# Optimization experiments

Hardware: AMD Instinct MI355X
Metric: run time of the kernel (lower is better)

The kernel has to match this reference:

```python
import jax, jax.numpy as jnp
import numpy as np

N = 20000   # nodes
E = 320000  # edges (before self loops)
B = 32      # graphs in batch
H = 4       # heads
C = 64      # per-head channels
NEG_SLOPE = 0.2


def setup_inputs() -> dict:
    key = jax.random.key(0)
    ks = jax.random.split(key, 16)
    x = jax.random.normal(ks[0], (N, 62), jnp.float32)
    pos = jax.random.uniform(ks[1], (N, 2), jnp.float32)
    edge_index = jax.random.randint(ks[2], (2, E), 0, N, jnp.int64)
    batch = jnp.sort(jax.random.randint(ks[3], (N,), 0, B, jnp.int64))
    def glorot(k, shape):
        fan = shape[0] + shape[-1]
        return jax.random.normal(k, shape, jnp.float32) * jnp.sqrt(2.0 / fan)
    # GAT layer 1: in 64 -> H*C = 256
    W1 = glorot(ks[4], (64, H * C))
    a_src1 = glorot(ks[5], (H, C))
    a_dst1 = glorot(ks[6], (H, C))
    b1 = jnp.zeros((H * C,), jnp.float32)
    # GAT layer 2: in 256 -> 256
    W2 = glorot(ks[7], (H * C, H * C))
    a_src2 = glorot(ks[8], (H, C))
    a_dst2 = glorot(ks[9], (H, C))
    b2 = jnp.zeros((H * C,), jnp.float32)
    # linear tail 256 -> 128 -> 10
    lw1 = glorot(ks[10], (H * C, 128))
    lb1 = jnp.zeros((128,), jnp.float32)
    lw2 = glorot(ks[11], (128, 10))
    lb2 = jnp.zeros((10,), jnp.float32)
    return {"x": x, "pos": pos, "edge_index": edge_index, "batch": batch,
            "W1": W1, "a_src1": a_src1, "a_dst1": a_dst1, "b1": b1,
            "W2": W2, "a_src2": a_src2, "a_dst2": a_dst2, "b2": b2,
            "lw1": lw1, "lb1": lb1, "lw2": lw2, "lb2": lb2}


def gat_layer(x, src, dst, W, a_src, a_dst, b):
    # x: [N, F_in] -> h: [N, H, C]
    h = (x @ W).reshape(N, H, C)
    alpha_s = jnp.einsum('nhc,hc->nh', h, a_src)  # [N,H]
    alpha_d = jnp.einsum('nhc,hc->nh', h, a_dst)
    e = alpha_s[src] + alpha_d[dst]               # [E',H]
    e = jax.nn.leaky_relu(e, NEG_SLOPE)
    # softmax over incoming edges per destination node
    emax = jax.ops.segment_max(e, dst, num_segments=N)  # every node has a self loop
    p = jnp.exp(e - emax[dst])
    denom = jax.ops.segment_sum(p, dst, num_segments=N)
    alpha = p / (denom[dst] + 1e-16)              # [E',H]
    msg = h[src] * alpha[..., None]               # [E',H,C] gather + weight
    out = jax.ops.segment_sum(msg, dst, num_segments=N)  # scatter-add
    return out.reshape(N, H * C) + b


def reference(x, pos, edge_index, batch, W1, a_src1, a_dst1, b1,
              W2, a_src2, a_dst2, b2, lw1, lb1, lw2, lb2):
    out = jnp.concatenate([pos, x], axis=1)       # [N, 64]
    loop = jnp.arange(N, dtype=edge_index.dtype)
    src = jnp.concatenate([edge_index[0], loop])  # add self loops (PyG default)
    dst = jnp.concatenate([edge_index[1], loop])
    out = gat_layer(out, src, dst, W1, a_src1, a_dst1, b1)
    out = gat_layer(out, src, dst, W2, a_src2, a_dst2, b2)
    # global mean pool per graph
    sums = jax.ops.segment_sum(out, batch, num_segments=B)
    cnt = jax.ops.segment_sum(jnp.ones((N, 1), out.dtype), batch, num_segments=B)
    out = sums / jnp.maximum(cnt, 1.0)            # [B, 256]
    # dropout(p=0.2) is identity in eval mode
    out = jax.nn.relu(out @ lw1 + lb1)
    out = jax.nn.relu(out @ lw2 + lb2)            # relu after every linear, incl. last (faithful)
    return out
```

## Files before the change

### kernel.cpp

```cpp
#include <hip/hip_runtime.h>
#include <hip/hip_bf16.h>
#include <math.h>

#define N_NODES 20000
#define N_EDGES 320000
#define N_EDGES_SL (N_EDGES + N_NODES)
#define NB 32
#define NH 4
#define HC 256
#define POOL_CH 20
#define DCAP 64

typedef short s16x8 __attribute__((ext_vector_type(8)));
typedef unsigned short u16x8 __attribute__((ext_vector_type(8)));
typedef float f32x4 __attribute__((ext_vector_type(4)));

__device__ __forceinline__ float bf2f(ushort u) {
    union { unsigned int i; float f; } v; v.i = ((unsigned int)u) << 16; return v.f;
}
__device__ __forceinline__ ushort f2bf(float f) {
    union { float f; unsigned int i; } v; v.f = f;
    unsigned int u = v.i;
    unsigned int r = (u + 0x7FFFu + ((u >> 16) & 1u)) >> 16;
    return (ushort)r;
}

#define NZERO (N_NODES + NB * HC)
#define PB_ZERO   ((NZERO + 255) / 256)
#define PB_CONCAT 5000
#define PB_TCONV1 64
#define PB_TCONV2 256
__global__ __launch_bounds__(256) void prep_kernel(const float* __restrict__ x,
                                                   const float* __restrict__ pos,
                                                   ushort* __restrict__ x0,
                                                   const float* __restrict__ W1,
                                                   ushort* __restrict__ Wt1,
                                                   const float* __restrict__ W2,
                                                   ushort* __restrict__ Wt2,
                                                   int* __restrict__ fillc,
                                                   float* __restrict__ poolsum,
                                                   const int* __restrict__ batch,
                                                   int* __restrict__ gstart) {
    int blk = blockIdx.x;
    if (blk < PB_ZERO) {
        int i = blk * 256 + threadIdx.x;
        if (i < N_NODES) fillc[i] = 0;
        else if (i < NZERO) poolsum[i - N_NODES] = 0.f;
    } else if (blk < PB_ZERO + PB_CONCAT) {
        int i = (blk - PB_ZERO) * 256 + threadIdx.x;
        int n = i >> 6, j = i & 63;
        float v = (j < 2) ? pos[n * 2 + j] : x[n * 62 + (j - 2)];
        x0[i] = f2bf(v);
    } else if (blk < PB_ZERO + PB_CONCAT + PB_TCONV1) {
        int i = (blk - PB_ZERO - PB_CONCAT) * 256 + threadIdx.x;
        int n = i >> 6, k = i & 63;
        Wt1[i] = f2bf(W1[k * 256 + n]);
    } else if (blk < PB_ZERO + PB_CONCAT + PB_TCONV1 + PB_TCONV2) {
        int i = (blk - PB_ZERO - PB_CONCAT - PB_TCONV1) * 256 + threadIdx.x;
        int n = i >> 8, k = i & 255;
        Wt2[i] = f2bf(W2[k * 256 + n]);
    } else {
        int t = threadIdx.x;
        if (t > NB) return;
        int lo = 0, hi = N_NODES;
        while (lo < hi) {
            int mid = (lo + hi) >> 1;
            if (batch[mid] < t) lo = mid + 1; else hi = mid;
        }
        gstart[t] = lo;
    }
}

#define PB_FILL ((N_EDGES_SL + 255) / 256)
template<int K, int KC, bool DOFILL>
__global__ __launch_bounds__(256) void mfma_gemm(const ushort* __restrict__ A,
                                                 const ushort* __restrict__ Bt,
                                                 ushort* __restrict__ C,
                                                 const float* __restrict__ a_src,
                                                 const float* __restrict__ a_dst,
                                                 float* __restrict__ asb,
                                                 float* __restrict__ adb,
                                                 const int* __restrict__ ei,
                                                 int* __restrict__ fillc,
                                                 int* __restrict__ srclist) {
    constexpr int KP = KC + 8;
    constexpr int GEMM_BLOCKS = 2 * ((N_NODES + 63) / 64);
    int t = blockIdx.x;
    if (DOFILL && t >= GEMM_BLOCKS) {
        int i = (t - GEMM_BLOCKS) * 256 + threadIdx.x;
        if (i < N_EDGES_SL) {
            int src, dst;
            if (i < N_EDGES) { src = ei[i]; dst = ei[N_EDGES + i]; }
            else             { src = i - N_EDGES; dst = src; }
            int slot = atomicAdd(&fillc[dst], 1);
            if (slot < DCAP) srclist[dst * DCAP + slot] = src;
        }
        return;
    }
    __shared__ __align__(16) ushort As[64 * KP];
    __shared__ __align__(16) ushort Bs[128 * KP];
    int tid = threadIdx.x;
    int col0 = (t & 1) * 128, row0 = (t >> 1) * 64;
    int wave = tid >> 6, lane = tid & 63;
    int mm = lane & 15, quad = lane >> 4;
    f32x4 acc[8] = {};

    for (int kc0 = 0; kc0 < K; kc0 += KC) {
        if (kc0) __syncthreads();
        constexpr int ITER_A = (64 * KC) / 2048;
        constexpr int ITER_B = (128 * KC) / 2048;
#pragma unroll
        for (int it = 0; it < ITER_A; ++it) {
            int f = it * 2048 + tid * 8;
            int r = f / KC, k = f - r * KC;
            uint4 av = make_uint4(0u, 0u, 0u, 0u);
            if (row0 + r < N_NODES) av = *(const uint4*)&A[(size_t)(row0 + r) * K + kc0 + k];
            *(uint4*)&As[r * KP + k] = av;
        }
#pragma unroll
        for (int it = 0; it < ITER_B; ++it) {
            int f = it * 2048 + tid * 8;
            int r = f / KC, k = f - r * KC;
            uint4 bv = *(const uint4*)&Bt[(size_t)(col0 + r) * K + kc0 + k];
            *(uint4*)&Bs[r * KP + k] = bv;
        }
        __syncthreads();
#pragma unroll
        for (int kt = 0; kt < KC / 32; ++kt) {
            s16x8 a = *(const s16x8*)&As[(wave * 16 + mm) * KP + kt * 32 + quad * 8];
#pragma unroll
            for (int nt = 0; nt < 8; ++nt) {
                s16x8 b = *(const s16x8*)&Bs[(nt * 16 + mm) * KP + kt * 32 + quad * 8];
                acc[nt] = __builtin_amdgcn_mfma_f32_16x16x32_bf16(a, b, acc[nt], 0, 0, 0);
            }
        }
    }
#pragma unroll
    for (int r = 0; r < 4; ++r) {
        int gr = row0 + wave * 16 + quad * 4 + r;
        bool ok = gr < N_NODES;
        float s1a = 0.f, s2a = 0.f, s1b = 0.f, s2b = 0.f;
#pragma unroll
        for (int nt = 0; nt < 8; ++nt) {
            int gc = col0 + nt * 16 + mm;
            float av = acc[nt][r];
            if (ok) C[(size_t)gr * HC + gc] = f2bf(av);
            float as_ = a_src[gc], ad_ = a_dst[gc];
            if (nt < 4) { s1a += av * as_; s2a += av * ad_; }
            else        { s1b += av * as_; s2b += av * ad_; }
        }
#pragma unroll
        for (int off = 1; off < 16; off <<= 1) {
            s1a += __shfl_xor(s1a, off); s2a += __shfl_xor(s2a, off);
            s1b += __shfl_xor(s1b, off); s2b += __shfl_xor(s2b, off);
        }
        if (mm == 0 && ok) {
            int hd = col0 >> 6;
            asb[gr * NH + hd] = s1a;     adb[gr * NH + hd] = s2a;
            asb[gr * NH + hd + 1] = s1b; adb[gr * NH + hd + 1] = s2b;
        }
    }
}

__global__ __launch_bounds__(256) void gather_kernel(const ushort* __restrict__ h,
                                                     const float* __restrict__ as_in,
                                                     const float* __restrict__ ad_in,
                                                     const int* __restrict__ fillc,
                                                     const int* __restrict__ srclist,
                                                     const float* __restrict__ bias,
                                                     ushort* __restrict__ out) {
    __shared__ float wls[4][DCAP][NH];
    __shared__ int   sls[4][DCAP];
    __shared__ float dls[4][NH];
    int wave = threadIdx.x >> 6;
    int node = blockIdx.x * 4 + wave;
    int lane = threadIdx.x & 63;
    if (node >= N_NODES) return;
    int start = node * DCAP;
    int deg = fillc[node];

    {
        int hh = lane >> 4;
        int el = lane & 15;
        float adv = ad_in[node * NH + hh];
        float den = 0.f;
        for (int c = 0; c < deg; c += 16) {
            int j = c + el;
            if (j < deg) {
                int s = srclist[start + j];
                float e = as_in[s * NH + hh] + adv;
                e = (e > 0.f) ? e : 0.2f * e;
                float p = __expf(e);
                den += p;
                wls[wave][j][hh] = p;
                if (hh == 0) sls[wave][j] = s;
            }
        }
#pragma unroll
        for (int off = 8; off; off >>= 1) den += __shfl_xor(den, off);
        if (el == 0) dls[wave][hh] = den;
    }

    int ph = lane >> 5;
    int sl = lane & 31;
    int hh8 = sl >> 3;
    float invden = 1.0f / (dls[wave][hh8] + 1e-16f);
    float acc[8] = {0.f, 0.f, 0.f, 0.f, 0.f, 0.f, 0.f, 0.f};
#pragma unroll 4
    for (int j = 0; j < deg; j += 2) {
        int jj = j + ph;
        float p = 0.f;
        int s = 0;
        if (jj < deg) {
            s = sls[wave][jj];
            p = wls[wave][jj][hh8];
        }
        u16x8 hv = *(const u16x8*)&h[(size_t)s * HC + sl * 8];
#pragma unroll
        for (int k = 0; k < 8; ++k) acc[k] += p * bf2f(hv[k]);
    }
#pragma unroll
    for (int k = 0; k < 8; ++k) acc[k] += __shfl_xor(acc[k], 32);
    if (ph == 0) {
        const float* bp = &bias[sl * 8];
        u16x8 o;
#pragma unroll
        for (int k = 0; k < 8; ++k) o[k] = f2bf(acc[k] * invden + bp[k]);
        *(u16x8*)&out[(size_t)node * HC + sl * 8] = o;
    }
}

__global__ __launch_bounds__(256) void gpool_kernel(const ushort* __restrict__ o2,
                                                    const int* __restrict__ gstart,
                                                    float* __restrict__ poolsum) {
    int b = blockIdx.x / POOL_CH, chunk = blockIdx.x % POOL_CH;
    int c = threadIdx.x;
    int s = gstart[b], e = gstart[b + 1];
    int cnt = e - s;
    int per = (cnt + POOL_CH - 1) / POOL_CH;
    int ns = s + chunk * per;
    int ne = min(ns + per, e);
    if (ns >= ne) return;
    float acc = 0.f;
    for (int n = ns; n < ne; ++n) acc += bf2f(o2[(size_t)n * HC + c]);
    atomicAdd(&poolsum[b * HC + c], acc);
}

__global__ __launch_bounds__(128) void tail_kernel(const float* __restrict__ poolsum,
                                                   const int* __restrict__ gstart,
                                                   const float* __restrict__ lw1,
                                                   const float* __restrict__ lb1,
                                                   const float* __restrict__ lw2,
                                                   const float* __restrict__ lb2,
                                                   float* __restrict__ out) {
    __shared__ float pm[HC];
    __shared__ float hid[128];
    int b = blockIdx.x, t = threadIdx.x;
    int cnt = gstart[b + 1] - gstart[b];
    float inv = 1.0f / (float)max(cnt, 1);
    pm[t] = poolsum[b * HC + t] * inv;
    pm[t + 128] = poolsum[b * HC + t + 128] * inv;
    __syncthreads();
    float s = lb1[t];
    for (int c = 0; c < HC; ++c) s += pm[c] * lw1[c * 128 + t];
    hid[t] = fmaxf(s, 0.f);
    __syncthreads();
    if (t < 10) {
        float s2 = lb2[t];
        for (int k = 0; k < 128; ++k) s2 += hid[k] * lw2[k * 10 + t];
        out[b * 10 + t] = fmaxf(s2, 0.f);
    }
}

extern "C" void kernel_launch(void* const* d_in, const int* in_sizes, int n_in,
                              void* d_out, int out_size, void* d_ws, size_t ws_size,
                              hipStream_t stream) {
    const float* x      = (const float*)d_in[0];
    const float* pos    = (const float*)d_in[1];
    const int*   ei     = (const int*)d_in[2];
    const int*   batch  = (const int*)d_in[3];
    const float* W1     = (const float*)d_in[4];
    const float* a_src1 = (const float*)d_in[5];
    const float* a_dst1 = (const float*)d_in[6];
    const float* b1     = (const float*)d_in[7];
    const float* W2     = (const float*)d_in[8];
    const float* a_src2 = (const float*)d_in[9];
    const float* a_dst2 = (const float*)d_in[10];
    const float* b2     = (const float*)d_in[11];
    const float* lw1    = (const float*)d_in[12];
    const float* lb1    = (const float*)d_in[13];
    const float* lw2    = (const float*)d_in[14];
    const float* lb2    = (const float*)d_in[15];
    float* out = (float*)d_out;

    char* ws = (char*)d_ws;
    size_t off = 0;
    auto alloc = [&](size_t bytes) -> void* {
        void* p = ws + off;
        off = (off + bytes + 255) & ~(size_t)255;
        return p;
    };
    int*    fillc   = (int*)alloc(N_NODES * 4);
    float*  poolsum = (float*)alloc(NB * HC * 4);
    int*    srclist = (int*)alloc((size_t)N_NODES * DCAP * 4);
    int*    gstart  = (int*)alloc((NB + 1) * 4);
    ushort* x0      = (ushort*)alloc((size_t)N_NODES * 64 * 2);
    ushort* Wt1     = (ushort*)alloc(256 * 64 * 2);
    ushort* Wt2     = (ushort*)alloc(256 * 256 * 2);
    ushort* hbuf    = (ushort*)alloc((size_t)N_NODES * HC * 2);
    ushort* o1      = (ushort*)alloc((size_t)N_NODES * HC * 2);
    float*  asb     = (float*)alloc((size_t)N_NODES * NH * 4);
    float*  adb     = (float*)alloc((size_t)N_NODES * NH * 4);
    ushort* o2 = o1;

    prep_kernel<<<PB_ZERO + PB_CONCAT + PB_TCONV1 + PB_TCONV2 + 1, 256, 0, stream>>>(
        x, pos, x0, W1, Wt1, W2, Wt2, fillc, poolsum, batch, gstart);

    const int GEMM_BLOCKS = 2 * ((N_NODES + 63) / 64);
    int ngrid = (N_NODES + 3) / 4;
    mfma_gemm<64, 64, true><<<GEMM_BLOCKS + PB_FILL, 256, 0, stream>>>(
        x0, Wt1, hbuf, a_src1, a_dst1, asb, adb, ei, fillc, srclist);
    gather_kernel<<<ngrid, 256, 0, stream>>>(hbuf, asb, adb, fillc, srclist, b1, o1);
    mfma_gemm<256, 128, false><<<GEMM_BLOCKS, 256, 0, stream>>>(
        o1, Wt2, hbuf, a_src2, a_dst2, asb, adb, ei, fillc, srclist);
    gather_kernel<<<ngrid, 256, 0, stream>>>(hbuf, asb, adb, fillc, srclist, b2, o2);
    gpool_kernel<<<NB * POOL_CH, HC, 0, stream>>>(o2, gstart, poolsum);
    tail_kernel<<<NB, 128, 0, stream>>>(poolsum, gstart, lw1, lb1, lw2, lb2, out);
}
```

Measured before the change: 199.1 us.

## Fuse input concat/bf16 cast into first GEMM and vectorize gather softmax

```diff
diff --git a/kernel.cpp b/kernel.cpp
--- a/kernel.cpp
+++ b/kernel.cpp
@@ -27,13 +27,9 @@
 
 #define NZERO (N_NODES + NB * HC)
 #define PB_ZERO   ((NZERO + 255) / 256)
-#define PB_CONCAT 5000
 #define PB_TCONV1 64
 #define PB_TCONV2 256
-__global__ __launch_bounds__(256) void prep_kernel(const float* __restrict__ x,
-                                                   const float* __restrict__ pos,
-                                                   ushort* __restrict__ x0,
-                                                   const float* __restrict__ W1,
+__global__ __launch_bounds__(256) void prep_kernel(const float* __restrict__ W1,
                                                    ushort* __restrict__ Wt1,
                                                    const float* __restrict__ W2,
                                                    ushort* __restrict__ Wt2,
@@ -46,17 +42,12 @@
         int i = blk * 256 + threadIdx.x;
         if (i < N_NODES) fillc[i] = 0;
         else if (i < NZERO) poolsum[i - N_NODES] = 0.f;
-    } else if (blk < PB_ZERO + PB_CONCAT) {
+    } else if (blk < PB_ZERO + PB_TCONV1) {
         int i = (blk - PB_ZERO) * 256 + threadIdx.x;
-        int n = i >> 6, j = i & 63;
-        float v = (j < 2) ? pos[n * 2 + j] : x[n * 62 + (j - 2)];
-        x0[i] = f2bf(v);
-    } else if (blk < PB_ZERO + PB_CONCAT + PB_TCONV1) {
-        int i = (blk - PB_ZERO - PB_CONCAT) * 256 + threadIdx.x;
         int n = i >> 6, k = i & 63;
         Wt1[i] = f2bf(W1[k * 256 + n]);
-    } else if (blk < PB_ZERO + PB_CONCAT + PB_TCONV1 + PB_TCONV2) {
-        int i = (blk - PB_ZERO - PB_CONCAT - PB_TCONV1) * 256 + threadIdx.x;
+    } else if (blk < PB_ZERO + PB_TCONV1 + PB_TCONV2) {
+        int i = (blk - PB_ZERO - PB_TCONV1) * 256 + threadIdx.x;
         int n = i >> 8, k = i & 255;
         Wt2[i] = f2bf(W2[k * 256 + n]);
     } else {
@@ -72,21 +63,21 @@
 }
 
 #define PB_FILL ((N_EDGES_SL + 255) / 256)
-template<int K, int KC, bool DOFILL>
-__global__ __launch_bounds__(256) void mfma_gemm(const ushort* __restrict__ A,
-                                                 const ushort* __restrict__ Bt,
-                                                 ushort* __restrict__ C,
-                                                 const float* __restrict__ a_src,
-                                                 const float* __restrict__ a_dst,
-                                                 float* __restrict__ asb,
-                                                 float* __restrict__ adb,
-                                                 const int* __restrict__ ei,
-                                                 int* __restrict__ fillc,
-                                                 int* __restrict__ srclist) {
-    constexpr int KP = KC + 8;
-    constexpr int GEMM_BLOCKS = 2 * ((N_NODES + 63) / 64);
+#define GEMM_BLOCKS (2 * ((N_NODES + 63) / 64))
+__global__ __launch_bounds__(256) void gemm1_kernel(const float* __restrict__ x,
+                                                    const float* __restrict__ pos,
+                                                    const ushort* __restrict__ Bt,
+                                                    ushort* __restrict__ C,
+                                                    const float* __restrict__ a_src,
+                                                    const float* __restrict__ a_dst,
+                                                    float* __restrict__ asb,
+                                                    float* __restrict__ adb,
+                                                    const int* __restrict__ ei,
+                                                    int* __restrict__ fillc,
+                                                    int* __restrict__ srclist) {
+    constexpr int KP = 72;
     int t = blockIdx.x;
-    if (DOFILL && t >= GEMM_BLOCKS) {
+    if (t >= GEMM_BLOCKS) {
         int i = (t - GEMM_BLOCKS) * 256 + threadIdx.x;
         if (i < N_EDGES_SL) {
             int src, dst;
@@ -105,12 +96,87 @@
     int mm = lane & 15, quad = lane >> 4;
     f32x4 acc[8] = {};
 
+#pragma unroll
+    for (int it = 0; it < 2; ++it) {
+        int f = it * 2048 + tid * 8;
+        int r = f >> 6, k0 = f & 63;
+        int gr = row0 + r;
+        u16x8 av = {};
+        if (gr < N_NODES) {
+#pragma unroll
+            for (int i = 0; i < 8; ++i) {
+                int k = k0 + i;
+                float v = (k < 2) ? pos[gr * 2 + k] : x[(size_t)gr * 62 + (k - 2)];
+                av[i] = f2bf(v);
+            }
+        }
+        *(u16x8*)&As[r * KP + k0] = av;
+    }
+#pragma unroll
+    for (int it = 0; it < 4; ++it) {
+        int f = it * 2048 + tid * 8;
+        int r = f >> 6, k = f & 63;
+        uint4 bv = *(const uint4*)&Bt[(size_t)(col0 + r) * 64 + k];
+        *(uint4*)&Bs[r * KP + k] = bv;
+    }
+    __syncthreads();
+#pragma unroll
+    for (int kt = 0; kt < 2; ++kt) {
+        s16x8 a = *(const s16x8*)&As[(wave * 16 + mm) * KP + kt * 32 + quad * 8];
+#pragma unroll
+        for (int nt = 0; nt < 8; ++nt) {
+            s16x8 b = *(const s16x8*)&Bs[(nt * 16 + mm) * KP + kt * 32 + quad * 8];
+            acc[nt] = __builtin_amdgcn_mfma_f32_16x16x32_bf16(a, b, acc[nt], 0, 0, 0);
+        }
+    }
+#pragma unroll
+    for (int r = 0; r < 4; ++r) {
+        int gr = row0 + wave * 16 + quad * 4 + r;
+        bool ok = gr < N_NODES;
+        float s1a = 0.f, s2a = 0.f, s1b = 0.f, s2b = 0.f;
+#pragma unroll
+        for (int nt = 0; nt < 8; ++nt) {
+            int gc = col0 + nt * 16 + mm;
+            float av = acc[nt][r];
+            if (ok) C[(size_t)gr * HC + gc] = f2bf(av);
+            float as_ = a_src[gc], ad_ = a_dst[gc];
+            if (nt < 4) { s1a += av * as_; s2a += av * ad_; }
+            else        { s1b += av * as_; s2b += av * ad_; }
+        }
+#pragma unroll
+        for (int off = 1; off < 16; off <<= 1) {
+            s1a += __shfl_xor(s1a, off); s2a += __shfl_xor(s2a, off);
+            s1b += __shfl_xor(s1b, off); s2b += __shfl_xor(s2b, off);
+        }
+        if (mm == 0 && ok) {
+            int hd = col0 >> 6;
+            asb[gr * NH + hd] = s1a;     adb[gr * NH + hd] = s2a;
+            asb[gr * NH + hd + 1] = s1b; adb[gr * NH + hd + 1] = s2b;
+        }
+    }
+}
+
+__global__ __launch_bounds__(256) void gemm2_kernel(const ushort* __restrict__ A,
+                                                    const ushort* __restrict__ Bt,
+                                                    ushort* __restrict__ C,
+                                                    const float* __restrict__ a_src,
+                                                    const float* __restrict__ a_dst,
+                                                    float* __restrict__ asb,
+                                                    float* __restrict__ adb) {
+    constexpr int K = 256, KC = 128, KP = KC + 8;
+    __shared__ __align__(16) ushort As[64 * KP];
+    __shared__ __align__(16) ushort Bs[128 * KP];
+    int tid = threadIdx.x;
+    int t = blockIdx.x;
+    int col0 = (t & 1) * 128, row0 = (t >> 1) * 64;
+    int wave = tid >> 6, lane = tid & 63;
+    int mm = lane & 15, quad = lane >> 4;
+    f32x4 acc[8] = {};
+
     for (int kc0 = 0; kc0 < K; kc0 += KC) {
         if (kc0) __syncthreads();
-        constexpr int ITER_A = (64 * KC) / 2048;
-        constexpr int ITER_B = (128 * KC) / 2048;
-#pragma unroll
-        for (int it = 0; it < ITER_A; ++it) {
+#pragma unroll
+        for (int it = 0; it < 4; ++it) {
             int f = it * 2048 + tid * 8;
             int r = f / KC, k = f - r * KC;
             uint4 av = make_uint4(0u, 0u, 0u, 0u);
@@ -118,7 +184,7 @@
             *(uint4*)&As[r * KP + k] = av;
         }
 #pragma unroll
-        for (int it = 0; it < ITER_B; ++it) {
+        for (int it = 0; it < 8; ++it) {
             int f = it * 2048 + tid * 8;
             int r = f / KC, k = f - r * KC;
             uint4 bv = *(const uint4*)&Bt[(size_t)(col0 + r) * K + kc0 + k];
@@ -171,40 +237,43 @@
                                                      ushort* __restrict__ out) {
     __shared__ float wls[4][DCAP][NH];
     __shared__ int   sls[4][DCAP];
-    __shared__ float dls[4][NH];
     int wave = threadIdx.x >> 6;
     int node = blockIdx.x * 4 + wave;
     int lane = threadIdx.x & 63;
     if (node >= N_NODES) return;
     int start = node * DCAP;
-    int deg = fillc[node];
-
+    int deg = min(fillc[node], DCAP);
+
+    f32x4 den4 = {};
     {
-        int hh = lane >> 4;
-        int el = lane & 15;
-        float adv = ad_in[node * NH + hh];
-        float den = 0.f;
-        for (int c = 0; c < deg; c += 16) {
-            int j = c + el;
-            if (j < deg) {
-                int s = srclist[start + j];
-                float e = as_in[s * NH + hh] + adv;
+        f32x4 adv4 = *(const f32x4*)&ad_in[node * NH];
+        f32x4 p4 = {};
+        if (lane < deg) {
+            int s = srclist[start + lane];
+            sls[wave][lane] = s;
+            f32x4 as4 = *(const f32x4*)&as_in[s * NH];
+#pragma unroll
+            for (int hh = 0; hh < NH; ++hh) {
+                float e = as4[hh] + adv4[hh];
                 e = (e > 0.f) ? e : 0.2f * e;
-                float p = __expf(e);
-                den += p;
-                wls[wave][j][hh] = p;
-                if (hh == 0) sls[wave][j] = s;
+                p4[hh] = __expf(e);
             }
-        }
-#pragma unroll
-        for (int off = 8; off; off >>= 1) den += __shfl_xor(den, off);
-        if (el == 0) dls[wave][hh] = den;
+            *(f32x4*)&wls[wave][lane][0] = p4;
+        }
+        den4 = p4;
+#pragma unroll
+        for (int off = 32; off; off >>= 1) {
+            den4[0] += __shfl_xor(den4[0], off);
+            den4[1] += __shfl_xor(den4[1], off);
+            den4[2] += __shfl_xor(den4[2], off);
+            den4[3] += __shfl_xor(den4[3], off);
+        }
     }
 
     int ph = lane >> 5;
     int sl = lane & 31;
     int hh8 = sl >> 3;
-    float invden = 1.0f / (dls[wave][hh8] + 1e-16f);
+    float invden = 1.0f / (den4[hh8] + 1e-16f);
     float acc[8] = {0.f, 0.f, 0.f, 0.f, 0.f, 0.f, 0.f, 0.f};
 #pragma unroll 4
     for (int j = 0; j < deg; j += 2) {
@@ -304,7 +373,6 @@
     float*  poolsum = (float*)alloc(NB * HC * 4);
     int*    srclist = (int*)alloc((size_t)N_NODES * DCAP * 4);
     int*    gstart  = (int*)alloc((NB + 1) * 4);
-    ushort* x0      = (ushort*)alloc((size_t)N_NODES * 64 * 2);
     ushort* Wt1     = (ushort*)alloc(256 * 64 * 2);
     ushort* Wt2     = (ushort*)alloc(256 * 256 * 2);
     ushort* hbuf    = (ushort*)alloc((size_t)N_NODES * HC * 2);
@@ -313,16 +381,15 @@
     float*  adb     = (float*)alloc((size_t)N_NODES * NH * 4);
     ushort* o2 = o1;
 
-    prep_kernel<<<PB_ZERO + PB_CONCAT + PB_TCONV1 + PB_TCONV2 + 1, 256, 0, stream>>>(
-        x, pos, x0, W1, Wt1, W2, Wt2, fillc, poolsum, batch, gstart);
-
-    const int GEMM_BLOCKS = 2 * ((N_NODES + 63) / 64);
+    prep_kernel<<<PB_ZERO + PB_TCONV1 + PB_TCONV2 + 1, 256, 0, stream>>>(
+        W1, Wt1, W2, Wt2, fillc, poolsum, batch, gstart);
+
     int ngrid = (N_NODES + 3) / 4;
-    mfma_gemm<64, 64, true><<<GEMM_BLOCKS + PB_FILL, 256, 0, stream>>>(
-        x0, Wt1, hbuf, a_src1, a_dst1, asb, adb, ei, fillc, srclist);
+    gemm1_kernel<<<GEMM_BLOCKS + PB_FILL, 256, 0, stream>>>(
+        x, pos, Wt1, hbuf, a_src1, a_dst1, asb, adb, ei, fillc, srclist);
     gather_kernel<<<ngrid, 256, 0, stream>>>(hbuf, asb, adb, fillc, srclist, b1, o1);
-    mfma_gemm<256, 128, false><<<GEMM_BLOCKS, 256, 0, stream>>>(
-        o1, Wt2, hbuf, a_src2, a_dst2, asb, adb, ei, fillc, srclist);
+    gemm2_kernel<<<GEMM_BLOCKS, 256, 0, stream>>>(
+        o1, Wt2, hbuf, a_src2, a_dst2, asb, adb);
     gather_kernel<<<ngrid, 256, 0, stream>>>(hbuf, asb, adb, fillc, srclist, b2, o2);
     gpool_kernel<<<NB * POOL_CH, HC, 0, stream>>>(o2, gstart, poolsum);
     tail_kernel<<<NB, 128, 0, stream>>>(poolsum, gstart, lw1, lb1, lw2, lb2, out);
```

Measured after the change: 196.9 us. Within noise of the previous version (-1.1%).
